# Optimization experiments

Measured on AMD Instinct MI355X. Metric: run time of the kernel, lower is better.

Reference implementation:

```python
import jax, jax.numpy as jnp
import numpy as np

EMPHASIS_FACTOR = 1.5
TOP_K_PERCENT = 0.2


def setup_inputs() -> dict:
    key = jax.random.key(0)
    k1, k2 = jax.random.split(key)
    B, S, D = 32, 8192, 256
    x = jax.random.normal(k1, (B, S, D), dtype=jnp.float32)
    W = jax.random.normal(k2, (D, 1), dtype=jnp.float32) * (1.0 / np.sqrt(D))
    b = jnp.zeros((1,), dtype=jnp.float32)
    return {"x": x, "W": W, "b": b}


def reference(x, W, b):
    B, S, D = x.shape
    # e = tanh(x @ W + b): [B, S, 1]
    e = jnp.tanh(jnp.einsum('bsd,do->bso', x, W) + b)
    # softmax over seq axis, squeeze -> [B, S]
    a = jax.nn.softmax(e, axis=1)[..., 0]
    # top-k selection: k = max(1, int(S * top_k_percent)), static under jit
    k = max(1, int(S * TOP_K_PERCENT))
    _, top_k_idx = jax.lax.top_k(a, k)  # [B, k]
    # mask of top-k positions (equiv to one_hot + reduce_max, but a direct scatter)
    mask = jnp.zeros((B, S), dtype=bool).at[jnp.arange(B)[:, None], top_k_idx].set(True)
    emphasized_a = jnp.where(mask, a * EMPHASIS_FACTOR, a)  # [B, S]
    # weighted sum over seq -> [B, D]
    summed_output = jnp.einsum('bsd,bs->bd', x, emphasized_a)
    return summed_output, emphasized_a
```

## Files before the change

kernel.cpp:

```cpp
#include <hip/hip_runtime.h>
#include <math.h>

#define BB 32
#define SS 8192
#define DD 256
#define K_SEL 1638
#define EMPH 1.5f
#define NCHUNK 64
#define ROWS_PER_BLOCK (SS / NCHUNK)
#define HBINS 2048
#define HCH 8

__device__ __forceinline__ unsigned monokey(float f) {
    unsigned u = __float_as_uint(f);
    return u ^ ((u & 0x80000000u) ? 0xFFFFFFFFu : 0x80000000u);
}

__global__ __launch_bounds__(1024) void k1_e_hist(const float* __restrict__ x,
                                                  const float* __restrict__ W,
                                                  const float* __restrict__ bias,
                                                  float* __restrict__ e_ws,
                                                  unsigned* __restrict__ hist_ws) {
    __shared__ unsigned hist[HBINS];
    const int tid = threadIdx.x;
    const int lane = tid & 63;
    const int wv = tid >> 6;
    for (int i = tid; i < HBINS; i += 1024) hist[i] = 0;

    const int b = blockIdx.x >> 3;
    const int ch = blockIdx.x & 7;
    const int row0 = ch * 1024;

    const float4* W4 = (const float4*)W;
    const int cg = lane & 15;
    const float4 w0 = W4[cg];
    const float4 w1 = W4[cg + 16];
    const float4 w2 = W4[cg + 32];
    const float4 w3 = W4[cg + 48];
    const float bias0 = bias[0];
    __syncthreads();

    const float* xb = x + (size_t)b * SS * DD;
    float* eb = e_ws + (size_t)b * SS;

    for (int it = 0; it < 16; it++) {
        const int r = row0 + (it * 16 + wv) * 4 + (lane >> 4);
        const float4* rp = (const float4*)(xb + (size_t)r * DD);
        float4 a0 = rp[cg];
        float4 a1 = rp[cg + 16];
        float4 a2 = rp[cg + 32];
        float4 a3 = rp[cg + 48];
        float p = a0.x * w0.x + a0.y * w0.y + a0.z * w0.z + a0.w * w0.w;
        p += a1.x * w1.x + a1.y * w1.y + a1.z * w1.z + a1.w * w1.w;
        p += a2.x * w2.x + a2.y * w2.y + a2.z * w2.z + a2.w * w2.w;
        p += a3.x * w3.x + a3.y * w3.y + a3.z * w3.z + a3.w * w3.w;
        p += __shfl_xor(p, 1, 64);
        p += __shfl_xor(p, 2, 64);
        p += __shfl_xor(p, 4, 64);
        p += __shfl_xor(p, 8, 64);
        if (cg == 0) {
            float e = tanhf(p + bias0);
            eb[r] = e;
            atomicAdd(&hist[monokey(e) >> 21], 1u);
        }
    }
    __syncthreads();
    unsigned* hout = hist_ws + (size_t)blockIdx.x * HBINS;
    for (int i = tid; i < HBINS; i += 1024) hout[i] = hist[i];
}

__global__ __launch_bounds__(1024) void k2_select(const float* __restrict__ e_ws,
                                                  const unsigned* __restrict__ hist_ws,
                                                  float* __restrict__ ea_out) {
    const int b = blockIdx.x;
    const int tid = threadIdx.x;
    const int lane = tid & 63;
    const int wid = tid >> 6;

    __shared__ float se[SS];
    __shared__ float wredf[16];
    __shared__ unsigned binTot[HBINS];
    __shared__ unsigned gsuf[256];
    __shared__ unsigned h7[128];
    __shared__ unsigned wcnt[16];
    __shared__ unsigned uvar[3];
    __shared__ float fvar[1];

    const float* eg = e_ws + (size_t)b * SS;
    float* og = ea_out + (size_t)b * SS;

    float lsum = 0.0f;
    #pragma unroll
    for (int i = 0; i < 8; i++) {
        int s = tid + i * 1024;
        float v = eg[s];
        se[s] = v;
        lsum += expf(v);
    }
    #pragma unroll
    for (int off = 32; off >= 1; off >>= 1)
        lsum += __shfl_xor(lsum, off, 64);
    if (lane == 0) wredf[wid] = lsum;

    unsigned c0 = 0, c1 = 0;
    for (int ch = 0; ch < HCH; ch++) {
        const unsigned* hc = hist_ws + ((size_t)(b * HCH + ch)) * HBINS;
        c0 += hc[2 * tid];
        c1 += hc[2 * tid + 1];
    }
    binTot[2 * tid] = c0;
    binTot[2 * tid + 1] = c1;
    __syncthreads();

    if (tid == 0) {
        float z = 0.0f;
        for (int w = 0; w < 16; w++) z += wredf[w];
        fvar[0] = 1.0f / z;
    }
    if (tid < 256) {
        unsigned g = 0;
        #pragma unroll
        for (int j = 0; j < 8; j++) g += binTot[tid * 8 + j];
        gsuf[tid] = g;
    }
    __syncthreads();
    for (int off = 1; off < 256; off <<= 1) {
        unsigned add = 0;
        if (tid < 256 && tid + off < 256) add = gsuf[tid + off];
        __syncthreads();
        if (tid < 256) gsuf[tid] += add;
        __syncthreads();
    }
    if (tid < 256) {
        unsigned above = (tid == 255) ? 0u : gsuf[tid + 1];
        if (above < K_SEL && K_SEL <= gsuf[tid]) {
            unsigned running = above;
            for (int j = 7; j >= 0; j--) {
                int bin = tid * 8 + j;
                unsigned c = binTot[bin];
                if (running < K_SEL && K_SEL <= running + c) {
                    uvar[0] = (unsigned)bin;
                    uvar[1] = K_SEL - running;
                    break;
                }
                running += c;
            }
        }
    }
    __syncthreads();
    unsigned prefix = uvar[0];
    unsigned kk = uvar[1];

    #pragma unroll
    for (int pass = 0; pass < 3; pass++) {
        const int shift = 14 - 7 * pass;
        if (tid < 128) h7[tid] = 0;
        __syncthreads();
        #pragma unroll
        for (int i = 0; i < 8; i++) {
            int s = tid + i * 1024;
            unsigned key = monokey(se[s]);
            if ((key >> (shift + 7)) == prefix)
                atomicAdd(&h7[(key >> shift) & 127u], 1u);
        }
        __syncthreads();
        for (int off = 1; off < 128; off <<= 1) {
            unsigned add = 0;
            if (tid < 128 && tid + off < 128) add = h7[tid + off];
            __syncthreads();
            if (tid < 128) h7[tid] += add;
            __syncthreads();
        }
        if (tid < 128) {
            unsigned above = (tid == 127) ? 0u : h7[tid + 1];
            if (above < kk && kk <= h7[tid]) {
                uvar[0] = (prefix << 7) | (unsigned)tid;
                uvar[1] = kk - above;
            }
        }
        __syncthreads();
        prefix = uvar[0];
        kk = uvar[1];
        __syncthreads();
    }
    const unsigned T = prefix;
    const unsigned r = kk;
    const float invZ = fvar[0];

    if (tid == 0) uvar[2] = 0;
    __syncthreads();
    for (int chunk = 0; chunk < 8; chunk++) {
        int s = chunk * 1024 + tid;
        float v = se[s];
        unsigned key = monokey(v);
        bool gt = key > T;
        bool eq = (key == T);
        unsigned long long bal = __ballot(eq);
        unsigned waveTot = (unsigned)__popcll(bal);
        unsigned myPref = (unsigned)__popcll(bal & ((1ull << lane) - 1ull));
        if (lane == 0) wcnt[wid] = waveTot;
        __syncthreads();
        unsigned base = uvar[2];
        for (int w = 0; w < wid; w++) base += wcnt[w];
        unsigned rank = base + myPref;
        bool sel = gt || (eq && rank < r);
        float a = expf(v) * invZ;
        og[s] = sel ? a * EMPH : a;
        __syncthreads();
        if (tid == 0) {
            unsigned t = uvar[2];
            for (int w = 0; w < 16; w++) t += wcnt[w];
            uvar[2] = t;
        }
        __syncthreads();
    }
}

__global__ __launch_bounds__(256) void k3_weighted_partial(const float* __restrict__ x,
                                                           const float* __restrict__ ea,
                                                           float* __restrict__ part) {
    const int blk = blockIdx.x;
    const int b = blk / NCHUNK;
    const int chunk = blk % NCHUNK;
    const int lane = threadIdx.x & 63;
    const int wid  = threadIdx.x >> 6;
    const float* xb = x + ((size_t)b * SS + (size_t)chunk * ROWS_PER_BLOCK) * DD;
    const float* ab = ea + (size_t)b * SS + (size_t)chunk * ROWS_PER_BLOCK;
    float4 acc = make_float4(0.f, 0.f, 0.f, 0.f);
    for (int rr = wid; rr < ROWS_PER_BLOCK; rr += 4) {
        float4 x4 = ((const float4*)(xb + (size_t)rr * DD))[lane];
        float a = ab[rr];
        acc.x += x4.x * a; acc.y += x4.y * a; acc.z += x4.z * a; acc.w += x4.w * a;
    }
    __shared__ float lds[4 * 256];
    ((float4*)lds)[wid * 64 + lane] = acc;
    __syncthreads();
    const int t = threadIdx.x;
    float v = lds[0 * 256 + t] + lds[1 * 256 + t] + lds[2 * 256 + t] + lds[3 * 256 + t];
    part[(size_t)blk * 256 + t] = v;
}

__global__ __launch_bounds__(256) void k4_reduce(const float* __restrict__ part,
                                                 float* __restrict__ out) {
    const int b = blockIdx.x;
    const int d = threadIdx.x;
    float s = 0.0f;
    for (int c = 0; c < NCHUNK; c++)
        s += part[((size_t)b * NCHUNK + c) * 256 + d];
    out[b * 256 + d] = s;
}

__global__ __launch_bounds__(256) void f1_dot_tanh(const float* __restrict__ x,
                                                   const float* __restrict__ W,
                                                   const float* __restrict__ bias,
                                                   float* __restrict__ e) {
    const int lane = threadIdx.x & 63;
    const int wib  = threadIdx.x >> 6;
    const int waveId = blockIdx.x * 4 + wib;
    const int totalWaves = gridDim.x * 4;
    const float4 w4 = ((const float4*)W)[lane];
    const float bias0 = bias[0];
    for (int row = waveId; row < BB * SS; row += totalWaves) {
        float4 x4 = ((const float4*)(x + (size_t)row * DD))[lane];
        float p = x4.x * w4.x + x4.y * w4.y + x4.z * w4.z + x4.w * w4.w;
        #pragma unroll
        for (int off = 32; off >= 1; off >>= 1)
            p += __shfl_xor(p, off, 64);
        if (lane == 0) e[row] = tanhf(p + bias0);
    }
}
__global__ __launch_bounds__(1024) void f2_softmax_topk(float* __restrict__ ea) {
    const int b = blockIdx.x;
    const int tid = threadIdx.x;
    const int lane = tid & 63;
    const int wid  = tid >> 6;
    __shared__ float se[SS];
    __shared__ float wredf[16];
    __shared__ unsigned hist[256];
    __shared__ unsigned ssum[256];
    __shared__ unsigned wcnt[16];
    __shared__ unsigned uvar[3];
    __shared__ float fvar[1];
    float* eg = ea + (size_t)b * SS;
    float lsum = 0.0f;
    #pragma unroll
    for (int i = 0; i < 8; i++) {
        int s = tid + i * 1024;
        float v = eg[s];
        se[s] = v;
        lsum += expf(v);
    }
    #pragma unroll
    for (int off = 32; off >= 1; off >>= 1)
        lsum += __shfl_xor(lsum, off, 64);
    if (lane == 0) wredf[wid] = lsum;
    __syncthreads();
    if (tid == 0) {
        float z = 0.0f;
        for (int w = 0; w < 16; w++) z += wredf[w];
        fvar[0] = 1.0f / z;
    }
    __syncthreads();
    const float invZ = fvar[0];
    unsigned kk = K_SEL;
    unsigned prefix = 0;
    for (int byte = 3; byte >= 0; byte--) {
        if (tid < 256) hist[tid] = 0;
        __syncthreads();
        #pragma unroll
        for (int i = 0; i < 8; i++) {
            unsigned key = monokey(se[tid + i * 1024]);
            bool active = (byte == 3) || ((key >> ((byte + 1) * 8)) == prefix);
            if (active) atomicAdd(&hist[(key >> (byte * 8)) & 0xFFu], 1u);
        }
        __syncthreads();
        if (tid < 256) ssum[tid] = hist[tid];
        __syncthreads();
        for (int off = 1; off < 256; off <<= 1) {
            unsigned add = 0;
            if (tid < 256 && tid + off < 256) add = ssum[tid + off];
            __syncthreads();
            if (tid < 256) ssum[tid] += add;
            __syncthreads();
        }
        if (tid < 256) {
            unsigned above = (tid == 255) ? 0u : ssum[tid + 1];
            if (above < kk && kk <= ssum[tid]) {
                uvar[0] = (unsigned)tid;
                uvar[1] = kk - above;
            }
        }
        __syncthreads();
        prefix = (prefix << 8) | uvar[0];
        kk = uvar[1];
        __syncthreads();
    }
    const unsigned T = prefix;
    const unsigned r = kk;
    if (tid == 0) uvar[2] = 0;
    __syncthreads();
    for (int chunk = 0; chunk < 8; chunk++) {
        int s = chunk * 1024 + tid;
        float v = se[s];
        unsigned key = monokey(v);
        bool gt = key > T;
        bool eq = (key == T);
        unsigned long long bal = __ballot(eq);
        unsigned waveTot = (unsigned)__popcll(bal);
        unsigned myPref = (unsigned)__popcll(bal & ((1ull << lane) - 1ull));
        if (lane == 0) wcnt[wid] = waveTot;
        __syncthreads();
        unsigned base = uvar[2];
        for (int w = 0; w < wid; w++) base += wcnt[w];
        bool sel = gt || (eq && (base + myPref) < r);
        float a = expf(v) * invZ;
        eg[s] = sel ? a * EMPH : a;
        __syncthreads();
        if (tid == 0) {
            unsigned t = uvar[2];
            for (int w = 0; w < 16; w++) t += wcnt[w];
            uvar[2] = t;
        }
        __syncthreads();
    }
}
__global__ __launch_bounds__(256) void f0_zero(float* __restrict__ p, int n) {
    int i = blockIdx.x * blockDim.x + threadIdx.x;
    if (i < n) p[i] = 0.0f;
}
__global__ __launch_bounds__(256) void f3_weighted_atomic(const float* __restrict__ x,
                                                          const float* __restrict__ ea,
                                                          float* __restrict__ out) {
    const int blk = blockIdx.x;
    const int b = blk / NCHUNK;
    const int chunk = blk % NCHUNK;
    const int lane = threadIdx.x & 63;
    const int wid  = threadIdx.x >> 6;
    const float* xb = x + ((size_t)b * SS + (size_t)chunk * ROWS_PER_BLOCK) * DD;
    const float* ab = ea + (size_t)b * SS + (size_t)chunk * ROWS_PER_BLOCK;
    float4 acc = make_float4(0.f, 0.f, 0.f, 0.f);
    for (int rr = wid; rr < ROWS_PER_BLOCK; rr += 4) {
        float4 x4 = ((const float4*)(xb + (size_t)rr * DD))[lane];
        float a = ab[rr];
        acc.x += x4.x * a; acc.y += x4.y * a; acc.z += x4.z * a; acc.w += x4.w * a;
    }
    __shared__ float lds[4 * 256];
    ((float4*)lds)[wid * 64 + lane] = acc;
    __syncthreads();
    const int t = threadIdx.x;
    float v = lds[0 * 256 + t] + lds[1 * 256 + t] + lds[2 * 256 + t] + lds[3 * 256 + t];
    atomicAdd(&out[b * 256 + t], v);
}

extern "C" void kernel_launch(void* const* d_in, const int* in_sizes, int n_in,
                              void* d_out, int out_size, void* d_ws, size_t ws_size,
                              hipStream_t stream) {
    (void)in_sizes; (void)n_in; (void)out_size;
    const float* x    = (const float*)d_in[0];
    const float* W    = (const float*)d_in[1];
    const float* bias = (const float*)d_in[2];
    float* out = (float*)d_out;
    float* sum_out = out;
    float* ea = out + BB * DD;

    const size_t e_bytes    = (size_t)BB * SS * sizeof(float);
    const size_t hist_bytes = (size_t)BB * HCH * HBINS * sizeof(unsigned);
    const size_t part_bytes = (size_t)BB * NCHUNK * 256 * sizeof(float);
    if (ws_size >= e_bytes + hist_bytes + part_bytes) {
        float* e_ws       = (float*)d_ws;
        unsigned* hist_ws = (unsigned*)((char*)d_ws + e_bytes);
        float* part       = (float*)((char*)d_ws + e_bytes + hist_bytes);
        k1_e_hist<<<BB * HCH, 1024, 0, stream>>>(x, W, bias, e_ws, hist_ws);
        k2_select<<<BB, 1024, 0, stream>>>(e_ws, hist_ws, ea);
        k3_weighted_partial<<<BB * NCHUNK, 256, 0, stream>>>(x, ea, part);
        k4_reduce<<<BB, 256, 0, stream>>>(part, sum_out);
    } else {
        f1_dot_tanh<<<4096, 256, 0, stream>>>(x, W, bias, ea);
        f2_softmax_topk<<<BB, 1024, 0, stream>>>(ea);
        if (ws_size >= part_bytes) {
            float* part = (float*)d_ws;
            k3_weighted_partial<<<BB * NCHUNK, 256, 0, stream>>>(x, ea, part);
            k4_reduce<<<BB, 256, 0, stream>>>(part, sum_out);
        } else {
            f0_zero<<<(BB * DD + 255) / 256, 256, 0, stream>>>(sum_out, BB * DD);
            f3_weighted_atomic<<<BB * NCHUNK, 256, 0, stream>>>(x, ea, sum_out);
        }
    }
}
```

Baseline: 417.5 us.

## Fuse unnormalized weighted sum into score pass and add sparse top-k correction

The first kernel now accumulates sum of exp(e)*x per row while it already has x in registers, so the second full read of x (a 256 MB tensor) is removed. The selection kernel records the indices of the selected top-k rows and writes 1/Z. A small gather kernel then adds the 0.5x emphasis correction over only the selected rows, and a final kernel combines the pieces. This trades one full pass over x for extra register pressure (16 accumulators per lane), an expf on every lane, an LDS reduction, and an irregular gather over about 20% of the rows.

Measured after the change: 403.6 us. -3.3%, faster.

```diff
diff --git a/kernel.cpp b/kernel.cpp
--- a/kernel.cpp
+++ b/kernel.cpp
@@ -6,22 +6,27 @@
 #define DD 256
 #define K_SEL 1638
 #define EMPH 1.5f
+#define HBINS 2048
+#define HCH 8
+#define IDX_STRIDE 1664
+#define K5_BLOCKS 8
+#define K5_SLICE 205
 #define NCHUNK 64
 #define ROWS_PER_BLOCK (SS / NCHUNK)
-#define HBINS 2048
-#define HCH 8
 
 __device__ __forceinline__ unsigned monokey(float f) {
     unsigned u = __float_as_uint(f);
     return u ^ ((u & 0x80000000u) ? 0xFFFFFFFFu : 0x80000000u);
 }
 
-__global__ __launch_bounds__(1024) void k1_e_hist(const float* __restrict__ x,
-                                                  const float* __restrict__ W,
-                                                  const float* __restrict__ bias,
-                                                  float* __restrict__ e_ws,
-                                                  unsigned* __restrict__ hist_ws) {
+__global__ __launch_bounds__(1024) void k1_e_hist_s1(const float* __restrict__ x,
+                                                     const float* __restrict__ W,
+                                                     const float* __restrict__ bias,
+                                                     float* __restrict__ e_ws,
+                                                     unsigned* __restrict__ hist_ws,
+                                                     float* __restrict__ s1part) {
     __shared__ unsigned hist[HBINS];
+    __shared__ float red[16 * 256];
     const int tid = threadIdx.x;
     const int lane = tid & 63;
     const int wv = tid >> 6;
@@ -42,6 +47,10 @@
 
     const float* xb = x + (size_t)b * SS * DD;
     float* eb = e_ws + (size_t)b * SS;
+
+    float acc[16];
+    #pragma unroll
+    for (int m = 0; m < 16; m++) acc[m] = 0.0f;
 
     for (int it = 0; it < 16; it++) {
         const int r = row0 + (it * 16 + wv) * 4 + (lane >> 4);
@@ -58,20 +67,47 @@
         p += __shfl_xor(p, 2, 64);
         p += __shfl_xor(p, 4, 64);
         p += __shfl_xor(p, 8, 64);
+        float ev = tanhf(p + bias0);
+        float w = expf(ev);
         if (cg == 0) {
-            float e = tanhf(p + bias0);
-            eb[r] = e;
-            atomicAdd(&hist[monokey(e) >> 21], 1u);
-        }
+            eb[r] = ev;
+            atomicAdd(&hist[monokey(ev) >> 21], 1u);
+        }
+        acc[0] += w * a0.x;  acc[1] += w * a0.y;  acc[2] += w * a0.z;  acc[3] += w * a0.w;
+        acc[4] += w * a1.x;  acc[5] += w * a1.y;  acc[6] += w * a1.z;  acc[7] += w * a1.w;
+        acc[8] += w * a2.x;  acc[9] += w * a2.y;  acc[10] += w * a2.z; acc[11] += w * a2.w;
+        acc[12] += w * a3.x; acc[13] += w * a3.y; acc[14] += w * a3.z; acc[15] += w * a3.w;
+    }
+    #pragma unroll
+    for (int m = 0; m < 16; m++) {
+        acc[m] += __shfl_xor(acc[m], 16, 64);
+        acc[m] += __shfl_xor(acc[m], 32, 64);
+    }
+    if (lane < 16) {
+        #pragma unroll
+        for (int m = 0; m < 16; m++) red[wv * 256 + lane * 16 + m] = acc[m];
     }
     __syncthreads();
     unsigned* hout = hist_ws + (size_t)blockIdx.x * HBINS;
     for (int i = tid; i < HBINS; i += 1024) hout[i] = hist[i];
+    if (tid < 256) {
+        const int d = tid;
+        const int q = d >> 6;
+        const int cg2 = (d >> 2) & 15;
+        const int j = d & 3;
+        const int m = q * 4 + j;
+        float s = 0.0f;
+        #pragma unroll
+        for (int w = 0; w < 16; w++) s += red[w * 256 + cg2 * 16 + m];
+        s1part[(size_t)blockIdx.x * DD + d] = s;
+    }
 }
 
 __global__ __launch_bounds__(1024) void k2_select(const float* __restrict__ e_ws,
                                                   const unsigned* __restrict__ hist_ws,
-                                                  float* __restrict__ ea_out) {
+                                                  float* __restrict__ ea_out,
+                                                  float* __restrict__ zinv,
+                                                  int* __restrict__ idx_ws) {
     const int b = blockIdx.x;
     const int tid = threadIdx.x;
     const int lane = tid & 63;
@@ -84,10 +120,12 @@
     __shared__ unsigned h7[128];
     __shared__ unsigned wcnt[16];
     __shared__ unsigned uvar[3];
+    __shared__ unsigned selCnt;
     __shared__ float fvar[1];
 
     const float* eg = e_ws + (size_t)b * SS;
     float* og = ea_out + (size_t)b * SS;
+    int* il = idx_ws + (size_t)b * IDX_STRIDE;
 
     float lsum = 0.0f;
     #pragma unroll
@@ -110,12 +148,14 @@
     }
     binTot[2 * tid] = c0;
     binTot[2 * tid + 1] = c1;
+    if (tid == 0) selCnt = 0;
     __syncthreads();
 
     if (tid == 0) {
         float z = 0.0f;
         for (int w = 0; w < 16; w++) z += wredf[w];
         fvar[0] = 1.0f / z;
+        zinv[b] = fvar[0];
     }
     if (tid < 256) {
         unsigned g = 0;
@@ -158,8 +198,7 @@
         __syncthreads();
         #pragma unroll
         for (int i = 0; i < 8; i++) {
-            int s = tid + i * 1024;
-            unsigned key = monokey(se[s]);
+            unsigned key = monokey(se[tid + i * 1024]);
             if ((key >> (shift + 7)) == prefix)
                 atomicAdd(&h7[(key >> shift) & 127u], 1u);
         }
@@ -202,10 +241,13 @@
         __syncthreads();
         unsigned base = uvar[2];
         for (int w = 0; w < wid; w++) base += wcnt[w];
-        unsigned rank = base + myPref;
-        bool sel = gt || (eq && rank < r);
+        bool sel = gt || (eq && (base + myPref) < r);
         float a = expf(v) * invZ;
         og[s] = sel ? a * EMPH : a;
+        if (sel) {
+            unsigned slot = atomicAdd(&selCnt, 1u);
+            il[slot] = s;
+        }
         __syncthreads();
         if (tid == 0) {
             unsigned t = uvar[2];
@@ -216,38 +258,47 @@
     }
 }
 
-__global__ __launch_bounds__(256) void k3_weighted_partial(const float* __restrict__ x,
-                                                           const float* __restrict__ ea,
-                                                           float* __restrict__ part) {
-    const int blk = blockIdx.x;
-    const int b = blk / NCHUNK;
-    const int chunk = blk % NCHUNK;
+__global__ __launch_bounds__(256) void k5_corr(const float* __restrict__ x,
+                                               const float* __restrict__ ea,
+                                               const int* __restrict__ idx_ws,
+                                               float* __restrict__ corr) {
+    const int b = blockIdx.x >> 3;
+    const int j = blockIdx.x & 7;
     const int lane = threadIdx.x & 63;
-    const int wid  = threadIdx.x >> 6;
-    const float* xb = x + ((size_t)b * SS + (size_t)chunk * ROWS_PER_BLOCK) * DD;
-    const float* ab = ea + (size_t)b * SS + (size_t)chunk * ROWS_PER_BLOCK;
+    const int wid = threadIdx.x >> 6;
+    const int lo = j * K5_SLICE;
+    const int hi = (lo + K5_SLICE < K_SEL) ? lo + K5_SLICE : K_SEL;
+    const int* il = idx_ws + (size_t)b * IDX_STRIDE;
+    const float* xb = x + (size_t)b * SS * DD;
+    const float* ab = ea + (size_t)b * SS;
     float4 acc = make_float4(0.f, 0.f, 0.f, 0.f);
-    for (int rr = wid; rr < ROWS_PER_BLOCK; rr += 4) {
-        float4 x4 = ((const float4*)(xb + (size_t)rr * DD))[lane];
-        float a = ab[rr];
-        acc.x += x4.x * a; acc.y += x4.y * a; acc.z += x4.z * a; acc.w += x4.w * a;
+    for (int t = lo + wid; t < hi; t += 4) {
+        int s = il[t];
+        float w = ab[s] * (1.0f / 3.0f);
+        float4 x4 = ((const float4*)(xb + (size_t)s * DD))[lane];
+        acc.x += w * x4.x; acc.y += w * x4.y; acc.z += w * x4.z; acc.w += w * x4.w;
     }
     __shared__ float lds[4 * 256];
     ((float4*)lds)[wid * 64 + lane] = acc;
     __syncthreads();
     const int t = threadIdx.x;
-    float v = lds[0 * 256 + t] + lds[1 * 256 + t] + lds[2 * 256 + t] + lds[3 * 256 + t];
-    part[(size_t)blk * 256 + t] = v;
-}
-
-__global__ __launch_bounds__(256) void k4_reduce(const float* __restrict__ part,
-                                                 float* __restrict__ out) {
+    float v = lds[t] + lds[256 + t] + lds[512 + t] + lds[768 + t];
+    corr[(size_t)blockIdx.x * DD + t] = v;
+}
+
+__global__ __launch_bounds__(256) void k6_final(const float* __restrict__ s1part,
+                                                const float* __restrict__ corr,
+                                                const float* __restrict__ zinv,
+                                                float* __restrict__ out) {
     const int b = blockIdx.x;
     const int d = threadIdx.x;
-    float s = 0.0f;
-    for (int c = 0; c < NCHUNK; c++)
-        s += part[((size_t)b * NCHUNK + c) * 256 + d];
-    out[b * 256 + d] = s;
+    float s1 = 0.0f;
+    #pragma unroll
+    for (int ch = 0; ch < HCH; ch++) s1 += s1part[((size_t)b * HCH + ch) * DD + d];
+    float c = 0.0f;
+    #pragma unroll
+    for (int j = 0; j < K5_BLOCKS; j++) c += corr[((size_t)b * K5_BLOCKS + j) * DD + d];
+    out[b * DD + d] = s1 * zinv[b] + c;
 }
 
 __global__ __launch_bounds__(256) void f1_dot_tanh(const float* __restrict__ x,
@@ -388,7 +439,7 @@
     ((float4*)lds)[wid * 64 + lane] = acc;
     __syncthreads();
     const int t = threadIdx.x;
-    float v = lds[0 * 256 + t] + lds[1 * 256 + t] + lds[2 * 256 + t] + lds[3 * 256 + t];
+    float v = lds[t] + lds[256 + t] + lds[512 + t] + lds[768 + t];
     atomicAdd(&out[b * 256 + t], v);
 }
 
@@ -405,25 +456,29 @@
 
     const size_t e_bytes    = (size_t)BB * SS * sizeof(float);
     const size_t hist_bytes = (size_t)BB * HCH * HBINS * sizeof(unsigned);
-    const size_t part_bytes = (size_t)BB * NCHUNK * 256 * sizeof(float);
-    if (ws_size >= e_bytes + hist_bytes + part_bytes) {
-        float* e_ws       = (float*)d_ws;
-        unsigned* hist_ws = (unsigned*)((char*)d_ws + e_bytes);
-        float* part       = (float*)((char*)d_ws + e_bytes + hist_bytes);
-        k1_e_hist<<<BB * HCH, 1024, 0, stream>>>(x, W, bias, e_ws, hist_ws);
-        k2_select<<<BB, 1024, 0, stream>>>(e_ws, hist_ws, ea);
-        k3_weighted_partial<<<BB * NCHUNK, 256, 0, stream>>>(x, ea, part);
-        k4_reduce<<<BB, 256, 0, stream>>>(part, sum_out);
+    const size_t s1_bytes   = (size_t)BB * HCH * DD * sizeof(float);
+    const size_t corr_bytes = (size_t)BB * K5_BLOCKS * DD * sizeof(float);
+    const size_t zinv_bytes = 128;
+    const size_t idx_bytes  = (size_t)BB * IDX_STRIDE * sizeof(int);
+    const size_t need = e_bytes + hist_bytes + s1_bytes + corr_bytes + zinv_bytes + idx_bytes;
+
+    if (ws_size >= need) {
+        char* p = (char*)d_ws;
+        float*    e_ws    = (float*)p;                 p += e_bytes;
+        unsigned* hist_ws = (unsigned*)p;              p += hist_bytes;
+        float*    s1part  = (float*)p;                 p += s1_bytes;
+        float*    corr    = (float*)p;                 p += corr_bytes;
+        float*    zinv    = (float*)p;                 p += zinv_bytes;
+        int*      idx_ws  = (int*)p;
+
+        k1_e_hist_s1<<<BB * HCH, 1024, 0, stream>>>(x, W, bias, e_ws, hist_ws, s1part);
+        k2_select<<<BB, 1024, 0, stream>>>(e_ws, hist_ws, ea, zinv, idx_ws);
+        k5_corr<<<BB * K5_BLOCKS, 256, 0, stream>>>(x, ea, idx_ws, corr);
+        k6_final<<<BB, 256, 0, stream>>>(s1part, corr, zinv, sum_out);
     } else {
         f1_dot_tanh<<<4096, 256, 0, stream>>>(x, W, bias, ea);
         f2_softmax_topk<<<BB, 1024, 0, stream>>>(ea);
-        if (ws_size >= part_bytes) {
-            float* part = (float*)d_ws;
-            k3_weighted_partial<<<BB * NCHUNK, 256, 0, stream>>>(x, ea, part);
-            k4_reduce<<<BB, 256, 0, stream>>>(part, sum_out);
-        } else {
-            f0_zero<<<(BB * DD + 255) / 256, 256, 0, stream>>>(sum_out, BB * DD);
-            f3_weighted_atomic<<<BB * NCHUNK, 256, 0, stream>>>(x, ea, sum_out);
-        }
-    }
-}
+        f0_zero<<<(BB * DD + 255) / 256, 256, 0, stream>>>(sum_out, BB * DD);
+        f3_weighted_atomic<<<BB * NCHUNK, 256, 0, stream>>>(x, ea, sum_out);
+    }
+}
```
